# Kernel optimization log

Measured on AMD Instinct MI355X. Metric: run time of the kernel, lower is better.

Reference implementation:

```python
import jax, jax.numpy as jnp
import numpy as np

EMB, H, KV, HD = 2048, 32, 8, 64
G = H // KV  # group size = 4
SEQ, B = 2048, 1
EPS = 1e-6


def rms_norm(x, scale):
    # fp32 RMSNorm over last dim, no bias/centering
    v = jnp.mean(x.astype(jnp.float32) ** 2, axis=-1, keepdims=True)
    return (x * jax.lax.rsqrt(v + EPS) * scale).astype(x.dtype)


def apply_rope(x, cos, sin):
    # x: [b, h, s, d]; cos/sin: [s, d]
    d2 = x.shape[-1] // 2
    x1, x2 = x[..., :d2], x[..., d2:]
    rot = jnp.concatenate((-x2, x1), axis=-1)
    return (x * cos[None, None] + rot * sin[None, None]).astype(x.dtype)


def setup_inputs() -> dict:
    key = jax.random.key(0)
    ks = jax.random.split(key, 6)
    x = jax.random.normal(ks[0], (B, SEQ, EMB), jnp.float32)
    mask = jnp.triu(jnp.ones((SEQ, SEQ), jnp.bool_), k=1)  # causal: True = masked
    inv_freq = 1.0 / (10000.0 ** (np.arange(0, HD, 2, dtype=np.float32) / HD))
    t = np.arange(SEQ, dtype=np.float32)
    ang = np.outer(t, inv_freq)  # [seq, hd/2]
    ang = np.concatenate([ang, ang], axis=-1)  # [seq, hd]
    cos = jnp.asarray(np.cos(ang), jnp.float32)
    sin = jnp.asarray(np.sin(ang), jnp.float32)
    s = 0.02
    Wq = jax.random.normal(ks[1], (EMB, H * HD), jnp.float32) * s
    Wk = jax.random.normal(ks[2], (EMB, KV * HD), jnp.float32) * s
    Wv = jax.random.normal(ks[3], (EMB, KV * HD), jnp.float32) * s
    Wo = jax.random.normal(ks[4], (H * HD, EMB), jnp.float32) * s
    q_scale = jnp.ones((HD,), jnp.float32)
    k_scale = jnp.ones((HD,), jnp.float32)
    return {"x": x, "mask": mask, "cos": cos, "sin": sin, "Wq": Wq, "Wk": Wk,
            "Wv": Wv, "Wo": Wo, "q_scale": q_scale, "k_scale": k_scale}


def reference(x, mask, cos, sin, Wq, Wk, Wv, Wo, q_scale, k_scale):
    b, s, _ = x.shape
    q = (x @ Wq).reshape(b, s, H, HD).transpose(0, 2, 1, 3)     # [b,h,s,d]
    k = (x @ Wk).reshape(b, s, KV, HD).transpose(0, 2, 1, 3)    # [b,kv,s,d]
    v = (x @ Wv).reshape(b, s, KV, HD).transpose(0, 2, 1, 3)
    q = rms_norm(q, q_scale)
    k = rms_norm(k, k_scale)
    q = apply_rope(q, cos, sin)
    k = apply_rope(k, cos, sin)
    # grouped heads: h = kv*G + g (matches repeat_interleave along head dim)
    qg = q.reshape(b, KV, G, s, HD)
    scores = jnp.einsum('bkgqd,bkld->bkgql', qg, k) / jnp.sqrt(jnp.float32(HD))
    scores = jnp.where(mask[None, None, None], -jnp.inf, scores)
    w = jax.nn.softmax(scores.astype(jnp.float32), axis=-1).astype(q.dtype)
    ctx = jnp.einsum('bkgql,bkld->bkgqd', w, v)                 # [b,kv,g,s,d]
    ctx = ctx.reshape(b, H, s, HD).transpose(0, 2, 1, 3).reshape(b, s, H * HD)
    return ctx @ Wo
```

## Files before the change

### kernel.cpp

```cpp
#include <hip/hip_runtime.h>
#include <stdint.h>

#define EMB 2048
#define NH 32
#define NKV 8
#define HD 64
#define SEQ 2048
#define QKV_N 3072

using u16 = unsigned short;
typedef __attribute__((ext_vector_type(8))) short bf16x8;
typedef __attribute__((ext_vector_type(4))) float f32x4;
typedef __attribute__((ext_vector_type(4))) unsigned short u16x4;

#define MFMA16(a, b, c) __builtin_amdgcn_mfma_f32_16x16x32_bf16(a, b, c, 0, 0, 0)
#define EXP2_C8 11.5415603f

__device__ inline u16 f2b(float f) {
  union { float f; unsigned u; } v; v.f = f;
  unsigned r = v.u + 0x7fffu + ((v.u >> 16) & 1u);
  return (u16)(r >> 16);
}
__device__ inline u16 f2b_fast(float f) {
  union { float f; unsigned u; } v; v.f = f;
  return (u16)((v.u + 0x8000u) >> 16);
}

__device__ inline void gload16(const void* g, void* l) {
  __builtin_amdgcn_global_load_lds(
      (const __attribute__((address_space(1))) void*)g,
      (__attribute__((address_space(3))) void*)l, 16, 0, 0);
}

__global__ void prep(const float* __restrict__ x, u16* __restrict__ xb,
                     const float* __restrict__ Wq, const float* __restrict__ Wk,
                     const float* __restrict__ Wv, const float* __restrict__ Wo,
                     u16* __restrict__ qkvT, u16* __restrict__ WoT) {
  int bx = blockIdx.x;
  if (bx >= 80) {
    int unit = (bx - 80) * 32 + blockIdx.y;
    int i = unit * 256 + threadIdx.x;
    float4 v = ((const float4*)x)[i];
    u16x4 o = { f2b(v.x), f2b(v.y), f2b(v.z), f2b(v.w) };
    ((u16x4*)xb)[i] = o;
    return;
  }
  __shared__ float t[64][65];
  int tx = threadIdx.x & 63, ty = threadIdx.x >> 6;
  int r0 = blockIdx.y * 64;
  const float* src; int C, c0, drow; u16* dst;
  if (bx < 32)      { src = Wq; C = 2048; c0 = bx * 64;        drow = bx * 64;        dst = qkvT; }
  else if (bx < 40) { src = Wk; C = 512;  c0 = (bx - 32) * 64; drow = bx * 64;        dst = qkvT; }
  else if (bx < 48) { src = Wv; C = 512;  c0 = (bx - 40) * 64; drow = bx * 64;        dst = qkvT; }
  else              { src = Wo; C = 2048; c0 = (bx - 48) * 64; drow = (bx - 48) * 64; dst = WoT; }
#pragma unroll
  for (int i = 0; i < 16; ++i) {
    int r = ty * 16 + i;
    t[r][tx] = src[(size_t)(r0 + r) * C + c0 + tx];
  }
  __syncthreads();
#pragma unroll
  for (int i = 0; i < 16; ++i) {
    int r = ty * 16 + i;
    dst[(size_t)(drow + r) * 2048 + r0 + tx] = f2b(t[tx][r]);
  }
}

template<int OUT_MODE>
__global__ __launch_bounds__(256, 2)
void gemm_bt(const u16* __restrict__ A, const u16* __restrict__ BT,
             float* __restrict__ Cp, int M, int N, int K, int nwgy,
             const float* __restrict__ cosT, const float* __restrict__ sinT,
             const float* __restrict__ qsc, const float* __restrict__ ksc,
             u16* __restrict__ qb, u16* __restrict__ kb, u16* __restrict__ vT) {
  __shared__ u16 As[2][64 * 64];
  __shared__ u16 Bs[2][128 * 64];
  const int tid = threadIdx.x;
  const int w = tid >> 6, lane = tid & 63;
  const int lr = lane & 15, lg = lane >> 4;
  const int nwg = gridDim.x, cpx = nwg >> 3, pos = blockIdx.x;
  const int o = (pos & 7) * cpx + (pos >> 3);
  const int by = o % nwgy, bx = o / nwgy;
  const int m0 = by * 64, n0 = bx * 128;
  const int wm = (w >> 1) * 32, wn = (w & 1) * 64;
  f32x4 acc[2][4] = {};
  const int nk = K >> 6;

  auto STAGE = [&](int buf, int kt) {
    const int k0 = kt << 6;
    const int j = tid & 7;
    const int rr = tid >> 3;
#pragma unroll
    for (int i = 0; i < 2; ++i) {
      int r = i * 32 + rr;
      int sc = (j ^ (r & 7)) * 8;
      gload16(&A[(size_t)(m0 + r) * K + k0 + sc], (char*)As[buf] + i * 4096 + w * 1024);
    }
#pragma unroll
    for (int i = 0; i < 4; ++i) {
      int r = i * 32 + rr;
      int sc = (j ^ (r & 7)) * 8;
      gload16(&BT[(size_t)(n0 + r) * K + k0 + sc], (char*)Bs[buf] + i * 4096 + w * 1024);
    }
  };

  int cur = 0;
  STAGE(0, 0);
  asm volatile("s_waitcnt vmcnt(0)" ::: "memory");
  __syncthreads();
  for (int kt = 0; kt < nk; ++kt) {
    if (kt + 1 < nk) STAGE(cur ^ 1, kt + 1);
#pragma unroll
    for (int ks = 0; ks < 2; ++ks) {
      bf16x8 a[2], b[4];
#pragma unroll
      for (int i = 0; i < 2; ++i) {
        int row = wm + i * 16 + lr;
        a[i] = *(const bf16x8*)&As[cur][row * 64 + ((ks * 4 + lg) ^ (row & 7)) * 8];
      }
#pragma unroll
      for (int j = 0; j < 4; ++j) {
        int row = wn + j * 16 + lr;
        b[j] = *(const bf16x8*)&Bs[cur][row * 64 + ((ks * 4 + lg) ^ (row & 7)) * 8];
      }
#pragma unroll
      for (int i = 0; i < 2; ++i)
#pragma unroll
        for (int j = 0; j < 4; ++j)
          acc[i][j] = MFMA16(a[i], b[j], acc[i][j]);
    }
    asm volatile("s_waitcnt vmcnt(0)" ::: "memory");
    __syncthreads();
    cur ^= 1;
  }

  if (OUT_MODE == 0) {
#pragma unroll
    for (int i = 0; i < 2; ++i)
#pragma unroll
      for (int j = 0; j < 4; ++j)
#pragma unroll
        for (int r = 0; r < 4; ++r) {
          int row = m0 + wm + i * 16 + lg * 4 + r;
          int col = n0 + wn + j * 16 + lr;
          Cp[(size_t)row * N + col] = acc[i][j][r];
        }
  } else {
    const int hh = (n0 + wn) >> 6;
    if (hh < 40) {
      const float* scp = (hh < 32) ? qsc : ksc;
      u16* dst = (hh < 32) ? (qb + (size_t)hh * SEQ * HD)
                           : (kb + (size_t)(hh - 32) * SEQ * HD);
      const float qmul = (hh < 32) ? 0.18033688f : 1.0f;
#pragma unroll
      for (int i = 0; i < 2; ++i)
#pragma unroll
        for (int r = 0; r < 4; ++r) {
          float ssq = 0.f;
#pragma unroll
          for (int j = 0; j < 4; ++j) ssq += acc[i][j][r] * acc[i][j][r];
          ssq += __shfl_xor(ssq, 1);
          ssq += __shfl_xor(ssq, 2);
          ssq += __shfl_xor(ssq, 4);
          ssq += __shfl_xor(ssq, 8);
          float rs = rsqrtf(ssq * (1.0f / 64.0f) + 1e-6f);
          int s = m0 + wm + i * 16 + lg * 4 + r;
          float xn[4];
#pragma unroll
          for (int j = 0; j < 4; ++j) xn[j] = acc[i][j][r] * rs * scp[j * 16 + lr];
#pragma unroll
          for (int j = 0; j < 2; ++j) {
            int d = j * 16 + lr;
            float o1 = (xn[j] * cosT[s * 64 + d] - xn[j + 2] * sinT[s * 64 + d]) * qmul;
            float o2 = (xn[j + 2] * cosT[s * 64 + 32 + d] + xn[j] * sinT[s * 64 + 32 + d]) * qmul;
            dst[(size_t)s * 64 + d] = f2b(o1);
            dst[(size_t)s * 64 + 32 + d] = f2b(o2);
          }
        }
    } else {
      const int kvh = hh - 40;
      const int sbase = m0 + wm + lg * 4;
#pragma unroll
      for (int i = 0; i < 2; ++i)
#pragma unroll
        for (int j = 0; j < 4; ++j) {
          int d = j * 16 + lr;
          u16x4 pk = { f2b(acc[i][j][0]), f2b(acc[i][j][1]),
                       f2b(acc[i][j][2]), f2b(acc[i][j][3]) };
          *(u16x4*)&vT[((size_t)kvh * HD + d) * SEQ + sbase + i * 16] = pk;
        }
    }
  }
}

template<bool MASKED>
__device__ __forceinline__ void attn_step(
    const u16* __restrict__ Ks, const u16* __restrict__ VTs, u16* __restrict__ Psw,
    bf16x8 q0, bf16x8 q1, f32x4* O, float* l_acc,
    int qbase, int kbase, int lr, int lg) {
  f32x4 sc[4];
#pragma unroll
  for (int kj = 0; kj < 4; ++kj) {
    int r2 = kj * 16 + lr, sw = r2 & 7;
    bf16x8 kf0 = *(const bf16x8*)&Ks[r2 * 64 + (lg ^ sw) * 8];
    bf16x8 kf1 = *(const bf16x8*)&Ks[r2 * 64 + ((4 + lg) ^ sw) * 8];
    f32x4 z = { -EXP2_C8, -EXP2_C8, -EXP2_C8, -EXP2_C8 };
    z = MFMA16(q0, kf0, z);
    z = MFMA16(q1, kf1, z);
    sc[kj] = z;
  }
#pragma unroll
  for (int kj = 0; kj < 4; ++kj)
#pragma unroll
    for (int r = 0; r < 4; ++r) {
      float p;
      if (MASKED) {
        int qg = qbase + lg * 4 + r;
        int kg = kbase + kj * 16 + lr;
        p = (kg > qg) ? 0.0f : exp2f(sc[kj][r]);
      } else {
        p = exp2f(sc[kj][r]);
      }
      l_acc[r] += p;
      int row = lg * 4 + r, col = kj * 16 + lr;
      int sj = (col >> 3) ^ (row & 7);
      Psw[row * 64 + sj * 8 + (col & 7)] = f2b_fast(p);
    }
#pragma unroll
  for (int ks2 = 0; ks2 < 2; ++ks2) {
    bf16x8 pa = *(const bf16x8*)&Psw[lr * 64 + ((ks2 * 4 + lg) ^ (lr & 7)) * 8];
#pragma unroll
    for (int n = 0; n < 4; ++n) {
      int r3 = n * 16 + lr, sw3 = r3 & 7;
      bf16x8 vb = *(const bf16x8*)&VTs[r3 * 64 + ((ks2 * 4 + lg) ^ sw3) * 8];
      O[n] = MFMA16(pa, vb, O[n]);
    }
  }
}

__global__ __launch_bounds__(256, 2)
void attn(const u16* __restrict__ qb, const u16* __restrict__ kb,
          const u16* __restrict__ vT, u16* __restrict__ ctx) {
  __shared__ u16 Ks[3][64 * 64];
  __shared__ u16 VTs[3][64 * 64];
  __shared__ u16 Ps[4][16 * 64];
  const int tid = threadIdx.x, w = tid >> 6, lane = tid & 63;
  const int lr = lane & 15, lg = lane >> 4;
  const int pos = blockIdx.x;
  const int o = (pos & 7) * 64 + (pos >> 3);
  const int h = o >> 4, p = o & 15;
  const int kvh = h >> 2;
  const int qtA = p, qtB = 31 - p;
  const int qbaseA = qtA * 64 + w * 16, qbaseB = qtB * 64 + w * 16;
  u16* Psw = &Ps[w][0];

  bf16x8 qA0 = *(const bf16x8*)&qb[((size_t)h * SEQ + qbaseA + lr) * HD + lg * 8];
  bf16x8 qA1 = *(const bf16x8*)&qb[((size_t)h * SEQ + qbaseA + lr) * HD + 32 + lg * 8];
  bf16x8 qB0 = *(const bf16x8*)&qb[((size_t)h * SEQ + qbaseB + lr) * HD + lg * 8];
  bf16x8 qB1 = *(const bf16x8*)&qb[((size_t)h * SEQ + qbaseB + lr) * HD + 32 + lg * 8];

  f32x4 OA[4] = {}, OB[4] = {};
  float lA[4] = {0.f, 0.f, 0.f, 0.f}, lB[4] = {0.f, 0.f, 0.f, 0.f};

  auto STAGE = [&](int buf, int kt) {
    const int kbase = kt * 64;
#pragma unroll
    for (int i = 0; i < 2; ++i) {
      int c = i * 256 + tid;
      int r = c >> 3, j = c & 7, sj = j ^ (r & 7);
      gload16(&kb[((size_t)kvh * SEQ + kbase + r) * HD + sj * 8],
              (char*)Ks[buf] + i * 4096 + w * 1024);
      gload16(&vT[((size_t)kvh * HD + r) * SEQ + kbase + sj * 8],
              (char*)VTs[buf] + i * 4096 + w * 1024);
    }
  };

  STAGE(0, 0);
  int cur = 0, nxt = 1;
  for (int kt = 0; kt <= qtB; ++kt) {
    if (kt < qtB) {
      STAGE(nxt, kt + 1);
      asm volatile("s_waitcnt vmcnt(4)" ::: "memory");
    } else {
      asm volatile("s_waitcnt vmcnt(0)" ::: "memory");
    }
    __builtin_amdgcn_s_barrier();
    const int kbase = kt * 64;
    if (kt <= qtA) {
      if (kt == qtA)
        attn_step<true >(Ks[cur], VTs[cur], Psw, qA0, qA1, OA, lA, qbaseA, kbase, lr, lg);
      else
        attn_step<false>(Ks[cur], VTs[cur], Psw, qA0, qA1, OA, lA, qbaseA, kbase, lr, lg);
    }
    if (kt == qtB)
      attn_step<true >(Ks[cur], VTs[cur], Psw, qB0, qB1, OB, lB, qbaseB, kbase, lr, lg);
    else
      attn_step<false>(Ks[cur], VTs[cur], Psw, qB0, qB1, OB, lB, qbaseB, kbase, lr, lg);
    cur = nxt;
    nxt = (nxt == 2) ? 0 : nxt + 1;
  }

#pragma unroll
  for (int r = 0; r < 4; ++r) {
#pragma unroll
    for (int off = 1; off < 16; off <<= 1) {
      lA[r] += __shfl_xor(lA[r], off);
      lB[r] += __shfl_xor(lB[r], off);
    }
  }
#pragma unroll
  for (int n = 0; n < 4; ++n)
#pragma unroll
    for (int r = 0; r < 4; ++r) {
      int sA = qbaseA + lg * 4 + r;
      ctx[(size_t)sA * 2048 + h * 64 + n * 16 + lr] = f2b(OA[n][r] / lA[r]);
      int sB = qbaseB + lg * 4 + r;
      ctx[(size_t)sB * 2048 + h * 64 + n * 16 + lr] = f2b(OB[n][r] / lB[r]);
    }
}

extern "C" void kernel_launch(void* const* d_in, const int* in_sizes, int n_in,
                              void* d_out, int out_size, void* d_ws, size_t ws_size,
                              hipStream_t stream) {
  const float* x    = (const float*)d_in[0];
  const float* cosT = (const float*)d_in[2];
  const float* sinT = (const float*)d_in[3];
  const float* Wq   = (const float*)d_in[4];
  const float* Wk   = (const float*)d_in[5];
  const float* Wv   = (const float*)d_in[6];
  const float* Wo   = (const float*)d_in[7];
  const float* qsc  = (const float*)d_in[8];
  const float* ksc  = (const float*)d_in[9];
  float* out = (float*)d_out;

  char* wsp = (char*)d_ws;
  u16*   xb    = (u16*)(wsp);
  u16*   WqkvT = (u16*)(wsp + ((size_t)8  << 20));
  u16*   WoT   = (u16*)(wsp + ((size_t)20 << 20));
  u16*   qbuf  = (u16*)(wsp + ((size_t)28 << 20));
  u16*   kbuf  = (u16*)(wsp + ((size_t)36 << 20));
  u16*   vTbuf = (u16*)(wsp + ((size_t)38 << 20));
  u16*   ctxb  = (u16*)(wsp + ((size_t)40 << 20));

  prep<<<dim3(208, 32), 256, 0, stream>>>(x, xb, Wq, Wk, Wv, Wo, WqkvT, WoT);

  gemm_bt<2><<<768, 256, 0, stream>>>(xb, WqkvT, nullptr, 2048, 3072, 2048, 32,
                                      cosT, sinT, qsc, ksc, qbuf, kbuf, vTbuf);
  attn<<<512, 256, 0, stream>>>(qbuf, kbuf, vTbuf, ctxb);
  gemm_bt<0><<<512, 256, 0, stream>>>((const u16*)ctxb, WoT, out, 2048, 2048, 2048, 32,
                                      nullptr, nullptr, nullptr, nullptr,
                                      nullptr, nullptr, nullptr);
}
```

Before: 124.8 us.

## Split attention KV range across two blocks and add combine kernel

Each attention work item (a pair of query tiles per head) is split into two halves of the key range, doubling the grid to 1024 blocks. Each half writes unnormalized bf16 partial outputs plus row sums to a workspace buffer, and a new combine kernel adds the two halves, normalizes, and transposes into the context layout. The attention kernel drops from triple to double buffering with an extra barrier and raises launch bounds to four blocks per CU. The goal is more parallelism and occupancy. The cost is an extra launch, roughly 16 MB of partial traffic, and bf16 rounding of the unnormalized partials.

```diff
diff --git a/kernel.cpp b/kernel.cpp
--- a/kernel.cpp
+++ b/kernel.cpp
@@ -24,6 +24,9 @@
 __device__ inline u16 f2b_fast(float f) {
   union { float f; unsigned u; } v; v.f = f;
   return (u16)((v.u + 0x8000u) >> 16);
+}
+__device__ inline float b2f(u16 u) {
+  union { unsigned u; float f; } v; v.u = ((unsigned)u) << 16; return v.f;
 }
 
 __device__ inline void gload16(const void* g, void* l) {
@@ -238,20 +241,24 @@
   }
 }
 
-__global__ __launch_bounds__(256, 2)
-void attn(const u16* __restrict__ qb, const u16* __restrict__ kb,
-          const u16* __restrict__ vT, u16* __restrict__ ctx) {
-  __shared__ u16 Ks[3][64 * 64];
-  __shared__ u16 VTs[3][64 * 64];
+__global__ __launch_bounds__(256, 4)
+void attn_sk(const u16* __restrict__ qb, const u16* __restrict__ kb,
+             const u16* __restrict__ vT, u16* __restrict__ Opart,
+             float* __restrict__ lpart) {
+  __shared__ u16 Ks[2][64 * 64];
+  __shared__ u16 VTs[2][64 * 64];
   __shared__ u16 Ps[4][16 * 64];
   const int tid = threadIdx.x, w = tid >> 6, lane = tid & 63;
   const int lr = lane & 15, lg = lane >> 4;
   const int pos = blockIdx.x;
-  const int o = (pos & 7) * 64 + (pos >> 3);
-  const int h = o >> 4, p = o & 15;
+  const int o = (pos & 7) * 128 + (pos >> 3);
+  const int h = o >> 5, p = (o >> 1) & 15, sh = o & 1;
   const int kvh = h >> 2;
   const int qtA = p, qtB = 31 - p;
   const int qbaseA = qtA * 64 + w * 16, qbaseB = qtB * 64 + w * 16;
+  const int mid = (qtB + 2) >> 1;
+  const int kt0 = sh ? mid : 0;
+  const int kt1 = sh ? qtB : (mid - 1);
   u16* Psw = &Ps[w][0];
 
   bf16x8 qA0 = *(const bf16x8*)&qb[((size_t)h * SEQ + qbaseA + lr) * HD + lg * 8];
@@ -275,11 +282,11 @@
     }
   };
 
-  STAGE(0, 0);
-  int cur = 0, nxt = 1;
-  for (int kt = 0; kt <= qtB; ++kt) {
-    if (kt < qtB) {
-      STAGE(nxt, kt + 1);
+  STAGE(0, kt0);
+  int cur = 0;
+  for (int kt = kt0; kt <= kt1; ++kt) {
+    if (kt < kt1) {
+      STAGE(cur ^ 1, kt + 1);
       asm volatile("s_waitcnt vmcnt(4)" ::: "memory");
     } else {
       asm volatile("s_waitcnt vmcnt(0)" ::: "memory");
@@ -296,8 +303,8 @@
       attn_step<true >(Ks[cur], VTs[cur], Psw, qB0, qB1, OB, lB, qbaseB, kbase, lr, lg);
     else
       attn_step<false>(Ks[cur], VTs[cur], Psw, qB0, qB1, OB, lB, qbaseB, kbase, lr, lg);
-    cur = nxt;
-    nxt = (nxt == 2) ? 0 : nxt + 1;
+    __builtin_amdgcn_s_barrier();
+    cur ^= 1;
   }
 
 #pragma unroll
@@ -308,15 +315,52 @@
       lB[r] += __shfl_xor(lB[r], off);
     }
   }
-#pragma unroll
-  for (int n = 0; n < 4; ++n)
+  const size_t baseA = ((size_t)(h * 32 + qtA) * 2 + sh) * 4096;
+  const size_t baseB = ((size_t)(h * 32 + qtB) * 2 + sh) * 4096;
+  const int rowb = w * 16 + lg * 4;
+#pragma unroll
+  for (int n = 0; n < 4; ++n) {
+    int col = n * 16 + lr;
+    u16x4 pa = { f2b(OA[n][0]), f2b(OA[n][1]), f2b(OA[n][2]), f2b(OA[n][3]) };
+    *(u16x4*)&Opart[baseA + (size_t)col * 64 + rowb] = pa;
+    u16x4 pb = { f2b(OB[n][0]), f2b(OB[n][1]), f2b(OB[n][2]), f2b(OB[n][3]) };
+    *(u16x4*)&Opart[baseB + (size_t)col * 64 + rowb] = pb;
+  }
+  if (lr == 0) {
+    const size_t lbA = ((size_t)(h * 32 + qtA) * 2 + sh) * 64;
+    const size_t lbB = ((size_t)(h * 32 + qtB) * 2 + sh) * 64;
 #pragma unroll
     for (int r = 0; r < 4; ++r) {
-      int sA = qbaseA + lg * 4 + r;
-      ctx[(size_t)sA * 2048 + h * 64 + n * 16 + lr] = f2b(OA[n][r] / lA[r]);
-      int sB = qbaseB + lg * 4 + r;
-      ctx[(size_t)sB * 2048 + h * 64 + n * 16 + lr] = f2b(OB[n][r] / lB[r]);
-    }
+      lpart[lbA + rowb + r] = lA[r];
+      lpart[lbB + rowb + r] = lB[r];
+    }
+  }
+}
+
+__global__ void combine(const u16* __restrict__ Opart, const float* __restrict__ lpart,
+                        u16* __restrict__ ctxb) {
+  __shared__ u16 tt[64][68];
+  __shared__ float invl[64];
+  const int h = blockIdx.x >> 5, qt = blockIdx.x & 31;
+  const int t = threadIdx.x;
+  const size_t b0 = ((size_t)(h * 32 + qt) * 2) * 4096;
+  const size_t lb = ((size_t)(h * 32 + qt) * 2) * 64;
+  if (t < 64) invl[t] = 1.0f / (lpart[lb + t] + lpart[lb + 64 + t]);
+  __syncthreads();
+#pragma unroll
+  for (int it = 0; it < 16; ++it) {
+    int e = it * 256 + t;
+    int col = e >> 6, row = e & 63;
+    float v = (b2f(Opart[b0 + e]) + b2f(Opart[b0 + 4096 + e])) * invl[row];
+    tt[row][col] = f2b(v);
+  }
+  __syncthreads();
+#pragma unroll
+  for (int it = 0; it < 16; ++it) {
+    int e = it * 256 + t;
+    int row = e >> 6, col = e & 63;
+    ctxb[(size_t)(qt * 64 + row) * 2048 + h * 64 + col] = tt[row][col];
+  }
 }
 
 extern "C" void kernel_launch(void* const* d_in, const int* in_sizes, int n_in,
@@ -336,17 +380,20 @@
   char* wsp = (char*)d_ws;
   u16*   xb    = (u16*)(wsp);
   u16*   WqkvT = (u16*)(wsp + ((size_t)8  << 20));
-  u16*   WoT   = (u16*)(wsp + ((size_t)20 << 20));
-  u16*   qbuf  = (u16*)(wsp + ((size_t)28 << 20));
-  u16*   kbuf  = (u16*)(wsp + ((size_t)36 << 20));
-  u16*   vTbuf = (u16*)(wsp + ((size_t)38 << 20));
+  u16*   Opart = (u16*)(wsp);
+  float* lpart = (float*)(wsp + ((size_t)16 << 20));
+  u16*   qbuf  = (u16*)(wsp + ((size_t)20 << 20));
+  u16*   kbuf  = (u16*)(wsp + ((size_t)28 << 20));
+  u16*   vTbuf = (u16*)(wsp + ((size_t)30 << 20));
+  u16*   WoT   = (u16*)(wsp + ((size_t)32 << 20));
   u16*   ctxb  = (u16*)(wsp + ((size_t)40 << 20));
 
   prep<<<dim3(208, 32), 256, 0, stream>>>(x, xb, Wq, Wk, Wv, Wo, WqkvT, WoT);
 
   gemm_bt<2><<<768, 256, 0, stream>>>(xb, WqkvT, nullptr, 2048, 3072, 2048, 32,
                                       cosT, sinT, qsc, ksc, qbuf, kbuf, vTbuf);
-  attn<<<512, 256, 0, stream>>>(qbuf, kbuf, vTbuf, ctxb);
+  attn_sk<<<1024, 256, 0, stream>>>(qbuf, kbuf, vTbuf, Opart, lpart);
+  combine<<<1024, 256, 0, stream>>>(Opart, lpart, ctxb);
   gemm_bt<0><<<512, 256, 0, stream>>>((const u16*)ctxb, WoT, out, 2048, 2048, 2048, 32,
                                       nullptr, nullptr, nullptr, nullptr,
                                       nullptr, nullptr, nullptr);
```

Measured after the change: 136.7 us. 9.6% more time.
